# Kernel tuning notes

Measured on AMD Instinct MI355X. Metric: run time of the kernel, lower is better.

The kernel has to match this reference:

```python
import jax, jax.numpy as jnp
import numpy as np

N_VOXELS = 150000
N_PAIRS = 60000   # rulebook pairs per kernel offset
K = 27            # 3x3x3 kernel offsets
CIN, COUT = 32, 64
BN_EPS = 1e-5


def setup_inputs() -> dict:
    key = jax.random.key(0)
    ks = jax.random.split(key, 5)
    features = jax.random.normal(ks[0], (N_VOXELS, CIN), dtype=jnp.float32)
    in_idx = jax.random.randint(ks[1], (K, N_PAIRS), 0, N_VOXELS, dtype=jnp.int32)
    out_idx = jax.random.randint(ks[2], (K, N_PAIRS), 0, N_VOXELS, dtype=jnp.int32)
    # Kaiming-ish init for conv weight [K, cin, cout]
    weight = jax.random.normal(ks[3], (K, CIN, COUT), dtype=jnp.float32) * (2.0 / (K * CIN)) ** 0.5
    bias = jax.random.normal(ks[4], (COUT,), dtype=jnp.float32) * 0.01
    gamma = jnp.ones((COUT,), dtype=jnp.float32)
    beta = jnp.zeros((COUT,), dtype=jnp.float32)
    return {"features": features, "in_idx": in_idx, "out_idx": out_idx,
            "weight": weight, "bias": bias, "gamma": gamma, "beta": beta}


def reference(features, in_idx, out_idx, weight, bias, gamma, beta):
    # --- sparse conv: rulebook gather-matmul-scatter ---
    gathered = features[in_idx]                           # [K, P, cin]
    contrib = jnp.einsum('kpc,kco->kpo', gathered, weight)  # [K, P, cout]
    out = jax.ops.segment_sum(contrib.reshape(-1, COUT),
                              out_idx.reshape(-1),
                              num_segments=N_VOXELS)       # [N, cout]
    out = out + bias
    # --- ReLU (note: module applies ReLU BEFORE BatchNorm1d) ---
    out = jax.nn.relu(out)
    # --- BatchNorm1d over active voxels (training-mode batch stats) ---
    mean = jnp.mean(out, axis=0)
    var = jnp.var(out, axis=0)
    out = (out - mean) * jax.lax.rsqrt(var + BN_EPS) * gamma + beta
    return out
```

## Files before the change

kernel.cpp:

```cpp
#include <hip/hip_runtime.h>


#define N_VOXELS 150000
#define NP 60000
#define NK 27
#define CIN 32
#define COUT 64
#define BN_EPS 1e-5f
#define NELEM (N_VOXELS * COUT)

#define RVOX 64
#define RSHIFT 6
#define NR ((N_VOXELS + RVOX - 1) / RVOX)
#define CAP 1024

#define WS_CNT   0
#define WS_STATS 4096
#define WS_LIST  8192

typedef int v16i __attribute__((ext_vector_type(16)));

__global__ __launch_bounds__(256) void build_buckets(
    const int* __restrict__ in_idx,
    const int* __restrict__ out_idx,
    int* __restrict__ ws)
{
    const int idx = blockIdx.x * 256 + threadIdx.x;
    if (idx >= NK * NP) return;
    const int k    = idx / NP;
    const int vout = out_idx[idx];
    const int vin  = in_idx[idx];
    const int r    = vout >> RSHIFT;
    const int slot = atomicAdd(&ws[WS_CNT + r], 1);
    if (slot < CAP)
        ws[WS_LIST + r * CAP + slot] = (k << 24) | (vin << RSHIFT) | (vout & (RVOX - 1));
}

__global__ __launch_bounds__(256, 6) void conv_gather(
    const float* __restrict__ features,
    const float* __restrict__ weight,
    const float* __restrict__ bias,
    const int* __restrict__ ws_i,
    float* __restrict__ out,
    float* __restrict__ stats)
{
    __shared__ float accum[RVOX * COUT];
    __shared__ int   kbin[CAP];
    __shared__ int   khist[NK];
    __shared__ int   koff[NK + 1];
    __shared__ int   kcur[NK];
    __shared__ float lsum[COUT];
    __shared__ float lsq[COUT];

    const int r    = blockIdx.x;
    const int tid  = threadIdx.x;
    const int lane = tid & 63;
    const int wid  = tid >> 6;

    int n = ws_i[WS_CNT + r];
    if (n > CAP) n = CAP;
    const int* list = ws_i + WS_LIST + (size_t)r * CAP;

    float4* acc4 = reinterpret_cast<float4*>(accum);
    for (int i = tid; i < RVOX * COUT / 4; i += 256) acc4[i] = float4{0.f, 0.f, 0.f, 0.f};
    if (tid < NK) khist[tid] = 0;
    if (tid < COUT) { lsum[tid] = 0.f; lsq[tid] = 0.f; }
    __syncthreads();

    for (int i = tid; i < n; i += 256) atomicAdd(&khist[list[i] >> 24], 1);
    __syncthreads();
    if (tid == 0) {
        int a = 0;
        for (int k = 0; k < NK; ++k) { koff[k] = a; kcur[k] = a; a += khist[k]; }
        koff[NK] = a;
    }
    __syncthreads();
    for (int i = tid; i < n; i += 256) {
        const int pk = list[i];
        kbin[atomicAdd(&kcur[pk >> 24], 1)] = pk;
    }
    __syncthreads();

    for (int k = 0; k < NK; ++k) {
        const int b0 = koff[k], b1 = koff[k + 1];
        if (b0 == b1) continue;

        float w[CIN];
        const float* wk = weight + k * (CIN * COUT) + lane;
#pragma unroll
        for (int c = 0; c < CIN; ++c) w[c] = wk[c * COUT];

        for (int j = b0 + wid; j < b1; j += 4) {
            const int pk  = __builtin_amdgcn_readfirstlane(kbin[j]);
            const int vin = (pk >> RSHIFT) & 0x3FFFF;
            const int lv  = pk & (RVOX - 1);
            const float* row = features + (size_t)vin * CIN;

            v16i ra, rb;
            asm volatile(
                "s_load_dwordx16 %0, %2, 0\n\t"
                "s_load_dwordx16 %1, %2, 64\n\t"
                "s_waitcnt lgkmcnt(0)"
                : "=&s"(ra), "=&s"(rb)
                : "s"(row));

            float acc = 0.f;
#pragma unroll
            for (int c = 0; c < 16; ++c)
                acc = fmaf(__int_as_float(ra[c]), w[c], acc);
#pragma unroll
            for (int c = 0; c < 16; ++c)
                acc = fmaf(__int_as_float(rb[c]), w[16 + c], acc);

            atomicAdd(&accum[lv * COUT + lane], acc);
        }
    }
    __syncthreads();

    const int v0 = r * RVOX;
    const int nv = (N_VOXELS - v0 < RVOX) ? (N_VOXELS - v0) : RVOX;
    const float b = bias[lane];
    float rs = 0.f, rq = 0.f;
    for (int i = tid; i < nv * COUT; i += 256) {
        float y = accum[i] + b;
        y = fmaxf(y, 0.f);
        out[(size_t)v0 * COUT + i] = y;
        rs += y;
        rq += y * y;
    }
    atomicAdd(&lsum[lane], rs);
    atomicAdd(&lsq[lane], rq);
    __syncthreads();
    if (tid < COUT) atomicAdd(&stats[tid], lsum[tid]);
    else if (tid < 2 * COUT) atomicAdd(&stats[tid], lsq[tid - COUT]);
}

__global__ __launch_bounds__(256) void bn_apply(
    float* __restrict__ buf,
    const float* __restrict__ stats,
    const float* __restrict__ gamma,
    const float* __restrict__ beta)
{
    const float inv_n = 1.f / (float)N_VOXELS;
    const int cg = (threadIdx.x & 15) * 4;
    float sc[4], sh[4];
#pragma unroll
    for (int j = 0; j < 4; ++j) {
        const int c = cg + j;
        const float mean = stats[c] * inv_n;
        const float var  = stats[COUT + c] * inv_n - mean * mean;
        sc[j] = gamma[c] * rsqrtf(var + BN_EPS);
        sh[j] = beta[c] - mean * sc[j];
    }
    const int tid    = blockIdx.x * 256 + threadIdx.x;
    const int stride = gridDim.x * 256;
    float4* buf4 = reinterpret_cast<float4*>(buf);
    for (int i = tid; i < NELEM / 4; i += stride) {
        float4 y = buf4[i];
        y.x = fmaf(y.x, sc[0], sh[0]);
        y.y = fmaf(y.y, sc[1], sh[1]);
        y.z = fmaf(y.z, sc[2], sh[2]);
        y.w = fmaf(y.w, sc[3], sh[3]);
        buf4[i] = y;
    }
}

extern "C" void kernel_launch(void* const* d_in, const int* in_sizes, int n_in,
                              void* d_out, int out_size, void* d_ws, size_t ws_size,
                              hipStream_t stream) {
    const float* features = (const float*)d_in[0];
    const int*   in_idx   = (const int*)d_in[1];
    const int*   out_idx  = (const int*)d_in[2];
    const float* weight   = (const float*)d_in[3];
    const float* bias     = (const float*)d_in[4];
    const float* gamma    = (const float*)d_in[5];
    const float* beta     = (const float*)d_in[6];
    float* out   = (float*)d_out;
    int*   ws    = (int*)d_ws;
    float* stats = (float*)d_ws + WS_STATS;

    hipMemsetAsync(d_ws, 0, (size_t)WS_LIST * sizeof(int), stream);

    build_buckets<<<(NK * NP + 255) / 256, 256, 0, stream>>>(in_idx, out_idx, ws);

    conv_gather<<<NR, 256, 0, stream>>>(features, weight, bias, ws, out, stats);

    bn_apply<<<2048, 256, 0, stream>>>(out, stats, gamma, beta);
}
```

Baseline: 882.8 us.

## Gather bf16 feature rows with two pairs per scalar load batch

```diff
diff --git a/kernel.cpp b/kernel.cpp
--- a/kernel.cpp
+++ b/kernel.cpp
@@ -8,6 +8,7 @@
 #define COUT 64
 #define BN_EPS 1e-5f
 #define NELEM (N_VOXELS * COUT)
+#define NFEAT (N_VOXELS * CIN)
 
 #define RVOX 64
 #define RSHIFT 6
@@ -17,8 +18,28 @@
 #define WS_CNT   0
 #define WS_STATS 4096
 #define WS_LIST  8192
+#define WS_FBF16 (WS_LIST + NR * CAP)
 
 typedef int v16i __attribute__((ext_vector_type(16)));
+
+__global__ __launch_bounds__(256) void cvt_bf16(
+    const float* __restrict__ features, unsigned int* __restrict__ fbf16_u32)
+{
+    const int tid    = blockIdx.x * 256 + threadIdx.x;
+    const int stride = gridDim.x * 256;
+    const float4* f4 = reinterpret_cast<const float4*>(features);
+    for (int i = tid; i < NFEAT / 4; i += stride) {
+        float4 v = f4[i];
+        unsigned int u0 = __float_as_uint(v.x), u1 = __float_as_uint(v.y);
+        unsigned int u2 = __float_as_uint(v.z), u3 = __float_as_uint(v.w);
+        u0 = (u0 + 0x7FFFu + ((u0 >> 16) & 1u)) >> 16;
+        u1 = (u1 + 0x7FFFu + ((u1 >> 16) & 1u)) >> 16;
+        u2 = (u2 + 0x7FFFu + ((u2 >> 16) & 1u)) >> 16;
+        u3 = (u3 + 0x7FFFu + ((u3 >> 16) & 1u)) >> 16;
+        fbf16_u32[i * 2]     = u0 | (u1 << 16);
+        fbf16_u32[i * 2 + 1] = u2 | (u3 << 16);
+    }
+}
 
 __global__ __launch_bounds__(256) void build_buckets(
     const int* __restrict__ in_idx,
@@ -33,11 +54,12 @@
     const int r    = vout >> RSHIFT;
     const int slot = atomicAdd(&ws[WS_CNT + r], 1);
     if (slot < CAP)
-        ws[WS_LIST + r * CAP + slot] = (k << 24) | (vin << RSHIFT) | (vout & (RVOX - 1));
+        __builtin_nontemporal_store((k << 24) | (vin << RSHIFT) | (vout & (RVOX - 1)),
+                                    &ws[WS_LIST + r * CAP + slot]);
 }
 
 __global__ __launch_bounds__(256, 6) void conv_gather(
-    const float* __restrict__ features,
+    const unsigned short* __restrict__ fbf16,
     const float* __restrict__ weight,
     const float* __restrict__ bias,
     const int* __restrict__ ws_i,
@@ -90,29 +112,43 @@
 #pragma unroll
         for (int c = 0; c < CIN; ++c) w[c] = wk[c * COUT];
 
-        for (int j = b0 + wid; j < b1; j += 4) {
-            const int pk  = __builtin_amdgcn_readfirstlane(kbin[j]);
-            const int vin = (pk >> RSHIFT) & 0x3FFFF;
-            const int lv  = pk & (RVOX - 1);
-            const float* row = features + (size_t)vin * CIN;
+        for (int j0 = b0 + wid * 2; j0 < b1; j0 += 8) {
+            const bool hasB = (j0 + 1 < b1);
+            const int  jB   = hasB ? (j0 + 1) : j0;
+            const int pkA = __builtin_amdgcn_readfirstlane(kbin[j0]);
+            const int pkB = __builtin_amdgcn_readfirstlane(kbin[jB]);
+            const int vinA = (pkA >> RSHIFT) & 0x3FFFF, lvA = pkA & (RVOX - 1);
+            const int vinB = (pkB >> RSHIFT) & 0x3FFFF, lvB = pkB & (RVOX - 1);
+            const unsigned short* rowA = fbf16 + (size_t)vinA * CIN;
+            const unsigned short* rowB = fbf16 + (size_t)vinB * CIN;
 
             v16i ra, rb;
             asm volatile(
                 "s_load_dwordx16 %0, %2, 0\n\t"
-                "s_load_dwordx16 %1, %2, 64\n\t"
+                "s_load_dwordx16 %1, %3, 0\n\t"
                 "s_waitcnt lgkmcnt(0)"
                 : "=&s"(ra), "=&s"(rb)
-                : "s"(row));
-
-            float acc = 0.f;
-#pragma unroll
-            for (int c = 0; c < 16; ++c)
-                acc = fmaf(__int_as_float(ra[c]), w[c], acc);
-#pragma unroll
-            for (int c = 0; c < 16; ++c)
-                acc = fmaf(__int_as_float(rb[c]), w[16 + c], acc);
-
-            atomicAdd(&accum[lv * COUT + lane], acc);
+                : "s"(rowA), "s"(rowB));
+
+            float accA = 0.f;
+#pragma unroll
+            for (int i = 0; i < 16; ++i) {
+                const unsigned int s = (unsigned int)ra[i];
+                accA = fmaf(__uint_as_float(s << 16),        w[2 * i],     accA);
+                accA = fmaf(__uint_as_float(s & 0xFFFF0000u), w[2 * i + 1], accA);
+            }
+            atomicAdd(&accum[lvA * COUT + lane], accA);
+
+            if (hasB) {
+                float accB = 0.f;
+#pragma unroll
+                for (int i = 0; i < 16; ++i) {
+                    const unsigned int s = (unsigned int)rb[i];
+                    accB = fmaf(__uint_as_float(s << 16),        w[2 * i],     accB);
+                    accB = fmaf(__uint_as_float(s & 0xFFFF0000u), w[2 * i + 1], accB);
+                }
+                atomicAdd(&accum[lvB * COUT + lane], accB);
+            }
         }
     }
     __syncthreads();
@@ -178,12 +214,16 @@
     float* out   = (float*)d_out;
     int*   ws    = (int*)d_ws;
     float* stats = (float*)d_ws + WS_STATS;
+    unsigned int*   fbf16_u32 = (unsigned int*)(ws + WS_FBF16);
+    const unsigned short* fbf16 = (const unsigned short*)(ws + WS_FBF16);
 
     hipMemsetAsync(d_ws, 0, (size_t)WS_LIST * sizeof(int), stream);
 
+    cvt_bf16<<<1024, 256, 0, stream>>>(features, fbf16_u32);
+
     build_buckets<<<(NK * NP + 255) / 256, 256, 0, stream>>>(in_idx, out_idx, ws);
 
-    conv_gather<<<NR, 256, 0, stream>>>(features, weight, bias, ws, out, stats);
+    conv_gather<<<NR, 256, 0, stream>>>(fbf16, weight, bias, ws, out, stats);
 
     bn_apply<<<2048, 256, 0, stream>>>(out, stats, gamma, beta);
 }
```

New measurement: 902.0 us. 2.2% more time.
